# Kernel optimization log

Measured on AMD Instinct MI355X. Metric: run time of the kernel, lower is better.

Reference implementation:

```python
import jax, jax.numpy as jnp
import numpy as np
import math

V, E, H, NL = 10000, 256, 512, 2
B, T = 64, 128


def _lstm_cell(x, h, c, Wih, Whh, b):
    # PyTorch gate order: i, f, g, o
    gates = x @ Wih.T + h @ Whh.T + b
    i, f, g, o = jnp.split(gates, 4, axis=-1)
    c = jax.nn.sigmoid(f) * c + jax.nn.sigmoid(i) * jnp.tanh(g)
    h = jax.nn.sigmoid(o) * jnp.tanh(c)
    return h, c


def _run_layer(xs, Wih, Whh, b):
    # xs: [T, B, D]; returns outputs [T, B, H] and final (h, c)
    Bn = xs.shape[1]
    h0 = jnp.zeros((Bn, H), xs.dtype)
    c0 = jnp.zeros((Bn, H), xs.dtype)

    def step(carry, x):
        h, c = carry
        h, c = _lstm_cell(x, h, c, Wih, Whh, b)
        return (h, c), h

    (hT, cT), ys = jax.lax.scan(step, (h0, c0), xs)
    return ys, hT, cT


def setup_inputs() -> dict:
    key = jax.random.key(0)
    ks = jax.random.split(key, 24)
    s = 0.05

    def n(k, shape):
        return jax.random.normal(k, shape, dtype=jnp.float32) * s

    inp = {
        "input_ids": jax.random.randint(ks[0], (B, T), 0, V),
        "my_attention_mask": jax.random.randint(ks[1], (B, T), 0, 2),
        "update_step": 1000,
        # encoder params
        "enc_embed": n(ks[2], (V, E)),
        "enc_Wih0": n(ks[3], (4 * H, E)),
        "enc_Whh0": n(ks[4], (4 * H, H)),
        "enc_b0": n(ks[5], (4 * H,)),
        "enc_Wih1": n(ks[6], (4 * H, H)),
        "enc_Whh1": n(ks[7], (4 * H, H)),
        "enc_b1": n(ks[8], (4 * H,)),
        # decoder params
        "dec_embed": n(ks[9], (V, E)),
        "dec_Wih0": n(ks[10], (4 * H, E)),
        "dec_Whh0": n(ks[11], (4 * H, H)),
        "dec_b0": n(ks[12], (4 * H,)),
        "dec_Wih1": n(ks[13], (4 * H, H)),
        "dec_Whh1": n(ks[14], (4 * H, H)),
        "dec_b1": n(ks[15], (4 * H,)),
        "dec_Wout": n(ks[16], (V, H)),
        "dec_bout": n(ks[17], (V,)),
    }
    return inp


def _forward(input_ids, my_attention_mask, update_step,
             enc_embed, enc_Wih0, enc_Whh0, enc_b0, enc_Wih1, enc_Whh1, enc_b1,
             dec_embed, dec_Wih0, dec_Whh0, dec_b0, dec_Wih1, dec_Whh1, dec_b1,
             dec_Wout, dec_bout):
    temp_ids = input_ids.T                      # [T, B]
    mask = my_attention_mask                    # [B, T]

    # ---- encoder: 2-layer LSTM over the full sequence ----
    emb = enc_embed[temp_ids]                   # [T, B, E]
    ys0, h0, c0 = _run_layer(emb, enc_Wih0, enc_Whh0, enc_b0)
    _, h1, c1 = _run_layer(ys0, enc_Wih1, enc_Whh1, enc_b1)

    def dec_step(carry, tok):
        dh0, dc0, dh1, dc1 = carry
        x = dec_embed[tok]                      # [B, E]
        dh0, dc0 = _lstm_cell(x, dh0, dc0, dec_Wih0, dec_Whh0, dec_b0)
        dh1, dc1 = _lstm_cell(dh0, dh1, dc1, dec_Wih1, dec_Whh1, dec_b1)
        out = dh1 @ dec_Wout.T + dec_bout       # [B, V]
        return (dh0, dc0, dh1, dc1), out

    _, dec_outs = jax.lax.scan(dec_step, (h0, c0, h1, c1), temp_ids[:-1])  # [T-1, B, V]

    # ---- mask-driven compaction: outputs[i, j] = dec_out at t where
    #      i = exclusive-cumsum of mask[j, :t]; unwritten slots stay random ----
    outputs = jax.random.uniform(jax.random.key(42), (T, B, V), dtype=jnp.float32)
    idx = jnp.cumsum(mask, axis=1) - mask       # exclusive cumsum, [B, T]
    write_i = jnp.where(mask[:, 1:] > 0, idx[:, 1:], T)   # OOB -> dropped
    vals = jnp.transpose(dec_outs, (1, 0, 2))   # [B, T-1, V]
    outputs = outputs.at[write_i, jnp.arange(B)[:, None]].set(vals, mode="drop")

    # ---- hard gumbel-softmax with straight-through ----
    temperature = max(0.5, math.exp(-0.003 * update_step))
    eps = 1e-20
    U = jax.random.uniform(jax.random.key(7), (T, B, V), dtype=jnp.float32)
    g = -jnp.log(-jnp.log(U + eps) + eps)
    y = jax.nn.softmax((outputs + g) / temperature, axis=-1)
    y_hard = jax.nn.one_hot(jnp.argmax(y, axis=-1), V, dtype=y.dtype)
    gs = jax.lax.stop_gradient(y_hard - y) + y  # [T, B, V]

    # ---- scatter back into padded layout: masked positions pull compacted
    #      gumbel onehots, unmasked positions get onehot(input id) ----
    gathered = gs[jnp.clip(idx, 0, T - 1), jnp.arange(B)[:, None]]  # [B, T, V]
    id_onehot = jax.nn.one_hot(input_ids, V, dtype=jnp.float32)     # [B, T, V]
    onehots = jnp.where((mask > 0)[:, :, None], gathered, id_onehot)
    return onehots.reshape(B * T, V)


def reference(input_ids, my_attention_mask, update_step,
              enc_embed, enc_Wih0, enc_Whh0, enc_b0, enc_Wih1, enc_Whh1, enc_b1,
              dec_embed, dec_Wih0, dec_Whh0, dec_b0, dec_Wih1, dec_Whh1, dec_b1,
              dec_Wout, dec_bout):
    return _forward(input_ids, my_attention_mask, update_step,
                    enc_embed, enc_Wih0, enc_Whh0, enc_b0, enc_Wih1, enc_Whh1, enc_b1,
                    dec_embed, dec_Wih0, dec_Whh0, dec_b0, dec_Wih1, dec_Whh1, dec_b1,
                    dec_Wout, dec_bout)
```

## Files before the change

### kernel.cpp

```cpp
#include <hip/hip_runtime.h>
#include <stdint.h>


typedef short bf16x8 __attribute__((ext_vector_type(8)));
typedef float f32x4 __attribute__((ext_vector_type(4)));

__device__ __forceinline__ void threefry2x32(uint32_t k0, uint32_t k1,
                                             uint32_t x0, uint32_t x1,
                                             uint32_t& o0, uint32_t& o1)
{
  const uint32_t k2 = k0 ^ k1 ^ 0x1BD11BDAu;
  x0 += k0; x1 += k1;
#define TF_R(r) x0 += x1; x1 = (x1 << r) | (x1 >> (32 - r)); x1 ^= x0;
  TF_R(13) TF_R(15) TF_R(26) TF_R(6)
  x0 += k1; x1 += k2 + 1u;
  TF_R(17) TF_R(29) TF_R(16) TF_R(24)
  x0 += k2; x1 += k0 + 2u;
  TF_R(13) TF_R(15) TF_R(26) TF_R(6)
  x0 += k0; x1 += k1 + 3u;
  TF_R(17) TF_R(29) TF_R(16) TF_R(24)
  x0 += k1; x1 += k2 + 4u;
  TF_R(13) TF_R(15) TF_R(26) TF_R(6)
  x0 += k2; x1 += k0 + 5u;
#undef TF_R
  o0 = x0; o1 = x1;
}

__device__ __forceinline__ float jax_uniform(uint32_t seed, uint32_t i)
{
  uint32_t o0, o1;
  threefry2x32(0u, seed, 0u, i, o0, o1);
  const uint32_t bits = o0 ^ o1;
  return __uint_as_float(0x3F800000u | (bits >> 9)) - 1.0f;
}

__device__ __forceinline__ ushort f2bf(float x)
{
  const uint32_t u = __float_as_uint(x);
  const uint32_t r = u + 0x7FFFu + ((u >> 16) & 1u);
  return (ushort)(r >> 16);
}
__device__ __forceinline__ float bf2f(ushort b)
{
  return __uint_as_float(((uint32_t)b) << 16);
}

__device__ __forceinline__ unsigned long long packkey(float f, int n)
{
  uint32_t u = __float_as_uint(f);
  u = (u & 0x80000000u) ? ~u : (u | 0x80000000u);
  return ((unsigned long long)u << 32) | (uint32_t)(0x7FFFFFFF - n);
}

__global__ __launch_bounds__(256)
void split_kernel(const float* __restrict__ src, ushort* __restrict__ hi,
                  ushort* __restrict__ lo, int n)
{
  const int i = blockIdx.x * 256 + threadIdx.x;
  if (i < n) {
    const float v = src[i];
    const ushort h = f2bf(v);
    hi[i] = h;
    lo[i] = f2bf(v - bf2f(h));
  }
}

__global__ __launch_bounds__(256)
void transpose_split_kernel(const float* __restrict__ seq,
                            ushort* __restrict__ Thi, ushort* __restrict__ Tlo)
{
  __shared__ float tile[128][65];
  const int t = blockIdx.x >> 2;
  const int kc = blockIdx.x & 3;
  const int tid = threadIdx.x;
  const float* sbase = seq + (size_t)t * 32768 + (size_t)kc * 128 * 64;
#pragma unroll
  for (int it = 0; it < 32; ++it) {
    const int idx = it * 256 + tid;
    tile[idx >> 6][idx & 63] = sbase[idx];
  }
  __syncthreads();
#pragma unroll
  for (int it = 0; it < 32; ++it) {
    const int idx = it * 256 + tid;
    const int b = idx >> 7, k = idx & 127;
    const float v = tile[k][b];
    const size_t o = ((size_t)t * 64 + b) * 512 + kc * 128 + k;
    const ushort h = f2bf(v);
    Thi[o] = h;
    Tlo[o] = f2bf(v - bf2f(h));
  }
}

template <int GATHER, int FUSED>
__global__ __launch_bounds__(256)
void gemm_split(const ushort* __restrict__ Ahi, const ushort* __restrict__ Alo,
                const int* __restrict__ ids,
                const ushort* __restrict__ Whi, const ushort* __restrict__ Wlo,
                const float* __restrict__ bias, float* __restrict__ Xg,
                const int* __restrict__ mask, const int* __restrict__ idxmap,
                unsigned long long* __restrict__ keys,
                int M, int N, int K)
{
  const int tid = threadIdx.x;
  const int wid = tid >> 6, lane = tid & 63;
  const int lm = lane & 15, quad = lane >> 4;
  const int m0 = blockIdx.x * 128 + (wid >> 1) * 64;
  const int n0 = blockIdx.y * 128 + (wid & 1) * 64;
  const int koff = quad * 8;

  size_t offA[4];
#pragma unroll
  for (int mi = 0; mi < 4; ++mi) {
    int m = m0 + mi * 16 + lm;
    int mc = m < M ? m : (M - 1);
    if (GATHER) {
      const int tok = ids[(mc & 63) * 128 + (mc >> 6)];
      offA[mi] = (size_t)tok * K;
    } else {
      offA[mi] = (size_t)mc * K;
    }
  }
  size_t offB[4];
#pragma unroll
  for (int ni = 0; ni < 4; ++ni) {
    int n = n0 + ni * 16 + lm;
    int nc = n < N ? n : (N - 1);
    offB[ni] = (size_t)nc * K;
  }

  f32x4 acc[4][4];
#pragma unroll
  for (int mi = 0; mi < 4; ++mi)
#pragma unroll
    for (int ni = 0; ni < 4; ++ni) acc[mi][ni] = (f32x4){0.f, 0.f, 0.f, 0.f};

  for (int k0 = 0; k0 < K; k0 += 32) {
    bf16x8 ah[4], al[4];
#pragma unroll
    for (int mi = 0; mi < 4; ++mi) {
      ah[mi] = *(const bf16x8*)(Ahi + offA[mi] + k0 + koff);
      al[mi] = *(const bf16x8*)(Alo + offA[mi] + k0 + koff);
    }
#pragma unroll
    for (int ni = 0; ni < 4; ++ni) {
      const bf16x8 bh = *(const bf16x8*)(Whi + offB[ni] + k0 + koff);
      const bf16x8 bl = *(const bf16x8*)(Wlo + offB[ni] + k0 + koff);
#pragma unroll
      for (int mi = 0; mi < 4; ++mi) {
        acc[mi][ni] = __builtin_amdgcn_mfma_f32_16x16x32_bf16(ah[mi], bl, acc[mi][ni], 0, 0, 0);
        acc[mi][ni] = __builtin_amdgcn_mfma_f32_16x16x32_bf16(al[mi], bh, acc[mi][ni], 0, 0, 0);
        acc[mi][ni] = __builtin_amdgcn_mfma_f32_16x16x32_bf16(ah[mi], bh, acc[mi][ni], 0, 0, 0);
      }
    }
  }

  float bv[4];
#pragma unroll
  for (int ni = 0; ni < 4; ++ni) {
    int n = n0 + ni * 16 + lm;
    bv[ni] = bias[n < N ? n : (N - 1)];
  }

  if (FUSED == 0) {
#pragma unroll
    for (int mi = 0; mi < 4; ++mi) {
#pragma unroll
      for (int i = 0; i < 4; ++i) {
        const int m = m0 + mi * 16 + quad * 4 + i;
        if (m >= M) continue;
        const int t = m >> 6, b = m & 63;
        float* base = Xg + (size_t)t * 131072 + b;
#pragma unroll
        for (int ni = 0; ni < 4; ++ni) {
          const int n = n0 + ni * 16 + lm;
          base[(size_t)n * 64] = acc[mi][ni][i] + bv[ni];
        }
      }
    }
  } else {
#pragma unroll
    for (int mi = 0; mi < 4; ++mi) {
#pragma unroll
      for (int i = 0; i < 4; ++i) {
        const int m = m0 + mi * 16 + quad * 4 + i;
        if (m >= M) continue;
        const int j = m >> 6, b = m & 63;
        const int outrow = b * 128 + j + 1;
        if (mask[outrow] == 0) continue;
        const int r = idxmap[outrow];
        const uint32_t base7 = (uint32_t)(r * 64 + b) * 10000u;
        float best = -3.0e38f;
        int bestn = 0;
#pragma unroll
        for (int ni = 0; ni < 4; ++ni) {
          const int n = n0 + ni * 16 + lm;
          if (n < N) {
            const float u7 = jax_uniform(7u, base7 + (uint32_t)n);
            const float g = -logf(-logf(u7 + 1e-20f) + 1e-20f);
            const float z = acc[mi][ni][i] + bv[ni] + g;
            if (z > best) { best = z; bestn = n; }
          }
        }
        unsigned long long key = packkey(best, bestn);
#pragma unroll
        for (int s = 1; s < 16; s <<= 1) {
          const unsigned long long o = __shfl_xor(key, s, 64);
          if (o > key) key = o;
        }
        if (lm == 0) atomicMax(keys + outrow, key);
      }
    }
  }
}

__global__ __launch_bounds__(128)
void lstm_step_kernel(const float* __restrict__ Xg,
                      const float* __restrict__ hprev,
                      const float* __restrict__ Whh,
                      float* __restrict__ cstate,
                      float* __restrict__ hout)
{
  __shared__ __align__(16) float ws[8][512];
  __shared__ __align__(16) float hs[4096];
  const int tid = threadIdx.x;
  const int b = tid & 63;
  const int ui = tid >> 6;
  const int U0 = blockIdx.x * 2;
  const int u = U0 + ui;

  {
    const int r = tid >> 4;
    const int lui = r >> 2, lg = r & 3;
    const float* wrow = Whh + (size_t)(lg * 512 + U0 + lui) * 512;
    const int kq = tid & 15;
#pragma unroll
    for (int i = 0; i < 8; ++i) {
      const int k = kq * 4 + i * 64;
      *(float4*)&ws[r][k] = *(const float4*)(wrow + k);
    }
  }

  const float x_i = Xg[(size_t)(0 * 512 + u) * 64 + b];
  const float x_f = Xg[(size_t)(1 * 512 + u) * 64 + b];
  const float x_g = Xg[(size_t)(2 * 512 + u) * 64 + b];
  const float x_o = Xg[(size_t)(3 * 512 + u) * 64 + b];
  const float c_old = cstate[(size_t)u * 64 + b];

  float4 pre[8];
#pragma unroll
  for (int i = 0; i < 8; ++i) pre[i] = ((const float4*)hprev)[tid + 128 * i];

  float a0 = 0.f, a1 = 0.f, a2 = 0.f, a3 = 0.f;
  for (int kc = 0; kc < 8; ++kc) {
    __syncthreads();
#pragma unroll
    for (int i = 0; i < 8; ++i) ((float4*)hs)[tid + 128 * i] = pre[i];
    __syncthreads();
    if (kc < 7) {
#pragma unroll
      for (int i = 0; i < 8; ++i)
        pre[i] = ((const float4*)hprev)[(kc + 1) * 1024 + tid + 128 * i];
    }
    const int kb = kc * 64;
#pragma unroll
    for (int kg = 0; kg < 16; ++kg) {
      const float h0 = hs[(kg * 4 + 0) * 64 + b];
      const float h1 = hs[(kg * 4 + 1) * 64 + b];
      const float h2 = hs[(kg * 4 + 2) * 64 + b];
      const float h3 = hs[(kg * 4 + 3) * 64 + b];
      const float4 w0 = *(const float4*)&ws[ui * 4 + 0][kb + kg * 4];
      const float4 w1 = *(const float4*)&ws[ui * 4 + 1][kb + kg * 4];
      const float4 w2 = *(const float4*)&ws[ui * 4 + 2][kb + kg * 4];
      const float4 w3 = *(const float4*)&ws[ui * 4 + 3][kb + kg * 4];
      a0 += h0 * w0.x + h1 * w0.y + h2 * w0.z + h3 * w0.w;
      a1 += h0 * w1.x + h1 * w1.y + h2 * w1.z + h3 * w1.w;
      a2 += h0 * w2.x + h1 * w2.y + h2 * w2.z + h3 * w2.w;
      a3 += h0 * w3.x + h1 * w3.y + h2 * w3.z + h3 * w3.w;
    }
  }

  const float zi = x_i + a0, zf = x_f + a1, zg = x_g + a2, zo = x_o + a3;
  const float I = 1.0f / (1.0f + expf(-zi));
  const float F = 1.0f / (1.0f + expf(-zf));
  const float G = tanhf(zg);
  const float O = 1.0f / (1.0f + expf(-zo));
  const float cn = F * c_old + I * G;
  cstate[(size_t)u * 64 + b] = cn;
  hout[(size_t)u * 64 + b] = O * tanhf(cn);
}

__global__ void maskscan_kernel(const int* __restrict__ mask,
                                int* __restrict__ idxmap)
{
  const int b = threadIdx.x;
  int run = 0;
  for (int t = 0; t < 128; ++t) {
    idxmap[b * 128 + t] = run;
    run += mask[b * 128 + t];
  }
}

__global__ __launch_bounds__(256)
void t0_kernel(const int* __restrict__ mask, unsigned long long* __restrict__ keys)
{
  const int b = blockIdx.x;
  const int row = b * 128;
  if (mask[row] == 0) return;
  const int tid = threadIdx.x;
  const uint32_t base = (uint32_t)b * 10000u;
  float best = -3.0e38f;
  int bestn = 0;
  for (int v = tid; v < 10000; v += 256) {
    const float u42 = jax_uniform(42u, base + (uint32_t)v);
    const float u7 = jax_uniform(7u, base + (uint32_t)v);
    const float g = -logf(-logf(u7 + 1e-20f) + 1e-20f);
    const float z = u42 + g;
    if (z > best) { best = z; bestn = v; }
  }
  __shared__ unsigned long long sk[256];
  sk[tid] = packkey(best, bestn);
  __syncthreads();
  for (int s = 128; s > 0; s >>= 1) {
    if (tid < s) { if (sk[tid + s] > sk[tid]) sk[tid] = sk[tid + s]; }
    __syncthreads();
  }
  if (tid == 0) keys[row] = sk[0];
}

__global__ __launch_bounds__(256)
void finalize_kernel(const unsigned long long* __restrict__ keys,
                     const int* __restrict__ mask,
                     const int* __restrict__ input_ids,
                     int* __restrict__ tokens)
{
  const int row = blockIdx.x * 256 + threadIdx.x;
  if (row < 8192) {
    tokens[row] = mask[row] ? (int)(0x7FFFFFFFu - (uint32_t)(keys[row] & 0xFFFFFFFFu))
                            : input_ids[row];
  }
}

__global__ __launch_bounds__(256)
void onehot_kernel(const int* __restrict__ tokens, float* __restrict__ out)
{
  const int row = blockIdx.x;
  const int tok = tokens[row];
  float4* orow = (float4*)(out + (size_t)row * 10000);
  for (int q = threadIdx.x; q < 2500; q += 256) {
    float4 v = make_float4(0.f, 0.f, 0.f, 0.f);
    const int v0 = q << 2;
    const unsigned d = (unsigned)(tok - v0);
    if (d < 4u) ((float*)&v)[d] = 1.0f;
    orow[q] = v;
  }
}

__global__ __launch_bounds__(256)
void zero_kernel(float* __restrict__ p, int n)
{
  const int i = blockIdx.x * 256 + threadIdx.x;
  if (i < n) p[i] = 0.f;
}

extern "C" void kernel_launch(void* const* d_in, const int* in_sizes, int n_in,
                              void* d_out, int out_size, void* d_ws, size_t ws_size,
                              hipStream_t stream)
{
  const int*   input_ids = (const int*)d_in[0];
  const int*   mask      = (const int*)d_in[1];
  const float* enc_embed = (const float*)d_in[3];
  const float* enc_Wih0  = (const float*)d_in[4];
  const float* enc_Whh0  = (const float*)d_in[5];
  const float* enc_b0    = (const float*)d_in[6];
  const float* enc_Wih1  = (const float*)d_in[7];
  const float* enc_Whh1  = (const float*)d_in[8];
  const float* enc_b1    = (const float*)d_in[9];
  const float* dec_embed = (const float*)d_in[10];
  const float* dec_Wih0  = (const float*)d_in[11];
  const float* dec_Whh0  = (const float*)d_in[12];
  const float* dec_b0    = (const float*)d_in[13];
  const float* dec_Wih1  = (const float*)d_in[14];
  const float* dec_Whh1  = (const float*)d_in[15];
  const float* dec_b1    = (const float*)d_in[16];
  const float* dec_Wout  = (const float*)d_in[17];
  const float* dec_bout  = (const float*)d_in[18];

  char* O = (char*)d_out;
  float*  Xg    = (float*)(O + 0);
  ushort* sThi  = (ushort*)(O + 67108864);
  ushort* sTlo  = (ushort*)(O + 75497472);
  ushort* eEh   = (ushort*)(O + 83886080);
  ushort* eEl   = (ushort*)(O + 89006080);
  ushort* dEh   = (ushort*)(O + 94126080);
  ushort* dEl   = (ushort*)(O + 99246080);
  ushort* eW0h  = (ushort*)(O + 104366080);
  ushort* eW0l  = (ushort*)(O + 105414656);
  ushort* eW1h  = (ushort*)(O + 106463232);
  ushort* eW1l  = (ushort*)(O + 108560384);
  ushort* dW0h  = (ushort*)(O + 110657536);
  ushort* dW0l  = (ushort*)(O + 111706112);
  ushort* dW1h  = (ushort*)(O + 112754688);
  ushort* dW1l  = (ushort*)(O + 114851840);
  ushort* Woh   = (ushort*)(O + 116948992);
  ushort* Wol   = (ushort*)(O + 127188992);
  unsigned long long* keys = (unsigned long long*)(O + 137428992);
  int*    idxmap = (int*)(O + 137494528);

  float* seqA = (float*)d_ws;
  float* zbuf = seqA + (size_t)128 * 32768;
  float* cA   = zbuf + 32768;
  float* cB   = cA + 32768;
  float* hp0  = cB + 32768;
  float* hp1  = hp0 + 32768;
  int* tokens = (int*)(hp1 + 32768);

  zero_kernel<<<384, 256, 0, stream>>>(zbuf, 3 * 32768);
  zero_kernel<<<64, 256, 0, stream>>>((float*)keys, 16384);
  maskscan_kernel<<<1, 64, 0, stream>>>(mask, idxmap);

  split_kernel<<<10000, 256, 0, stream>>>(enc_embed, eEh, eEl, 2560000);
  split_kernel<<<10000, 256, 0, stream>>>(dec_embed, dEh, dEl, 2560000);
  split_kernel<<<2048, 256, 0, stream>>>(enc_Wih0, eW0h, eW0l, 524288);
  split_kernel<<<4096, 256, 0, stream>>>(enc_Wih1, eW1h, eW1l, 1048576);
  split_kernel<<<2048, 256, 0, stream>>>(dec_Wih0, dW0h, dW0l, 524288);
  split_kernel<<<4096, 256, 0, stream>>>(dec_Wih1, dW1h, dW1l, 1048576);
  split_kernel<<<20000, 256, 0, stream>>>(dec_Wout, Woh, Wol, 5120000);

  gemm_split<1, 0><<<dim3(64, 16), 256, 0, stream>>>(
      eEh, eEl, input_ids, eW0h, eW0l, enc_b0, Xg,
      nullptr, nullptr, nullptr, 8192, 2048, 256);
  for (int t = 0; t < 128; ++t) {
    const float* hi = (t == 0) ? zbuf : (seqA + (size_t)(t - 1) * 32768);
    lstm_step_kernel<<<256, 128, 0, stream>>>(
        Xg + (size_t)t * 131072, hi, enc_Whh0, cA, seqA + (size_t)t * 32768);
  }

  transpose_split_kernel<<<512, 256, 0, stream>>>(seqA, sThi, sTlo);
  gemm_split<0, 0><<<dim3(64, 16), 256, 0, stream>>>(
      sThi, sTlo, nullptr, eW1h, eW1l, enc_b1, Xg,
      nullptr, nullptr, nullptr, 8192, 2048, 512);
  for (int t = 0; t < 128; ++t) {
    const float* hi = (t == 0) ? zbuf : ((t & 1) ? hp0 : hp1);
    float* ho = (t & 1) ? hp1 : hp0;
    lstm_step_kernel<<<256, 128, 0, stream>>>(
        Xg + (size_t)t * 131072, hi, enc_Whh1, cB, ho);
  }

  gemm_split<1, 0><<<dim3(64, 16), 256, 0, stream>>>(
      dEh, dEl, input_ids, dW0h, dW0l, dec_b0, Xg,
      nullptr, nullptr, nullptr, 8128, 2048, 256);
  for (int j = 0; j < 127; ++j) {
    const float* hi = (j == 0) ? (seqA + (size_t)127 * 32768)
                               : (seqA + (size_t)(j - 1) * 32768);
    lstm_step_kernel<<<256, 128, 0, stream>>>(
        Xg + (size_t)j * 131072, hi, dec_Whh0, cA, seqA + (size_t)j * 32768);
  }

  transpose_split_kernel<<<508, 256, 0, stream>>>(seqA, sThi, sTlo);
  gemm_split<0, 0><<<dim3(64, 16), 256, 0, stream>>>(
      sThi, sTlo, nullptr, dW1h, dW1l, dec_b1, Xg,
      nullptr, nullptr, nullptr, 8128, 2048, 512);
  for (int j = 0; j < 127; ++j) {
    const float* hi = (j == 0) ? hp1 : (seqA + (size_t)(j - 1) * 32768);
    lstm_step_kernel<<<256, 128, 0, stream>>>(
        Xg + (size_t)j * 131072, hi, dec_Whh1, cB, seqA + (size_t)j * 32768);
  }

  transpose_split_kernel<<<508, 256, 0, stream>>>(seqA, sThi, sTlo);
  gemm_split<0, 1><<<dim3(64, 79), 256, 0, stream>>>(
      sThi, sTlo, nullptr, Woh, Wol, dec_bout, nullptr,
      mask, idxmap, keys, 8128, 10000, 512);
  t0_kernel<<<64, 256, 0, stream>>>(mask, keys);

  finalize_kernel<<<32, 256, 0, stream>>>(keys, mask, input_ids, tokens);
  onehot_kernel<<<8192, 256, 0, stream>>>(tokens, (float*)d_out);
}
```

Baseline: 12.06 ms.

## Replace FP32 LSTM recurrent step with split-bf16 MFMA kernel using ping-pong hidden buffers

The recurrent h@Whh product in each LSTM timestep moves from an FP32 shared-memory dot-product kernel to a kernel using bf16 MFMA with a hi/lo split (three MFMAs per tile) to keep near-FP32 accuracy. Whh matrices are pre-split into bf16 hi/lo once, and each step writes its hidden state in a batch-major bf16 hi/lo layout into ping-pong buffers read by the next step. The kernel uses 32 blocks of 256 threads instead of 256 blocks of 128, so far fewer workgroups are used per step, which reduces parallelism across the GPU. There are also extra split launches and an extra per-step write of the hidden state.

```diff
diff --git a/kernel.cpp b/kernel.cpp
--- a/kernel.cpp
+++ b/kernel.cpp
@@ -214,80 +214,80 @@
   }
 }
 
-__global__ __launch_bounds__(128)
-void lstm_step_kernel(const float* __restrict__ Xg,
-                      const float* __restrict__ hprev,
-                      const float* __restrict__ Whh,
-                      float* __restrict__ cstate,
-                      float* __restrict__ hout)
-{
-  __shared__ __align__(16) float ws[8][512];
-  __shared__ __align__(16) float hs[4096];
+__global__ __launch_bounds__(256)
+void lstm_step_mfma(const float* __restrict__ Xg,
+                    const ushort* __restrict__ hHi, const ushort* __restrict__ hLo,
+                    const ushort* __restrict__ WHi, const ushort* __restrict__ WLo,
+                    float* __restrict__ cstate, float* __restrict__ hout,
+                    ushort* __restrict__ oHi, ushort* __restrict__ oLo)
+{
   const int tid = threadIdx.x;
-  const int b = tid & 63;
-  const int ui = tid >> 6;
-  const int U0 = blockIdx.x * 2;
-  const int u = U0 + ui;
-
-  {
-    const int r = tid >> 4;
-    const int lui = r >> 2, lg = r & 3;
-    const float* wrow = Whh + (size_t)(lg * 512 + U0 + lui) * 512;
-    const int kq = tid & 15;
-#pragma unroll
-    for (int i = 0; i < 8; ++i) {
-      const int k = kq * 4 + i * 64;
-      *(float4*)&ws[r][k] = *(const float4*)(wrow + k);
+  const int mi = tid >> 6;
+  const int lane = tid & 63;
+  const int lm = lane & 15, quad = lane >> 4;
+  const int u = blockIdx.x * 16 + lm;
+  const int koff = quad * 8;
+
+  const ushort* aHi = hHi + (size_t)(mi * 16 + lm) * 512 + koff;
+  const ushort* aLo = hLo + (size_t)(mi * 16 + lm) * 512 + koff;
+  const ushort* bH[4];
+  const ushort* bL[4];
+#pragma unroll
+  for (int g = 0; g < 4; ++g) {
+    const size_t o = (size_t)(g * 512 + u) * 512 + koff;
+    bH[g] = WHi + o;
+    bL[g] = WLo + o;
+  }
+
+  f32x4 acc[4];
+#pragma unroll
+  for (int g = 0; g < 4; ++g) acc[g] = (f32x4){0.f, 0.f, 0.f, 0.f};
+
+#pragma unroll 4
+  for (int k0 = 0; k0 < 512; k0 += 32) {
+    const bf16x8 ah = *(const bf16x8*)(aHi + k0);
+    const bf16x8 al = *(const bf16x8*)(aLo + k0);
+#pragma unroll
+    for (int g = 0; g < 4; ++g) {
+      const bf16x8 bh = *(const bf16x8*)(bH[g] + k0);
+      const bf16x8 bl = *(const bf16x8*)(bL[g] + k0);
+      acc[g] = __builtin_amdgcn_mfma_f32_16x16x32_bf16(ah, bl, acc[g], 0, 0, 0);
+      acc[g] = __builtin_amdgcn_mfma_f32_16x16x32_bf16(al, bh, acc[g], 0, 0, 0);
+      acc[g] = __builtin_amdgcn_mfma_f32_16x16x32_bf16(ah, bh, acc[g], 0, 0, 0);
     }
   }
 
-  const float x_i = Xg[(size_t)(0 * 512 + u) * 64 + b];
-  const float x_f = Xg[(size_t)(1 * 512 + u) * 64 + b];
-  const float x_g = Xg[(size_t)(2 * 512 + u) * 64 + b];
-  const float x_o = Xg[(size_t)(3 * 512 + u) * 64 + b];
-  const float c_old = cstate[(size_t)u * 64 + b];
-
-  float4 pre[8];
-#pragma unroll
-  for (int i = 0; i < 8; ++i) pre[i] = ((const float4*)hprev)[tid + 128 * i];
-
-  float a0 = 0.f, a1 = 0.f, a2 = 0.f, a3 = 0.f;
-  for (int kc = 0; kc < 8; ++kc) {
-    __syncthreads();
-#pragma unroll
-    for (int i = 0; i < 8; ++i) ((float4*)hs)[tid + 128 * i] = pre[i];
-    __syncthreads();
-    if (kc < 7) {
-#pragma unroll
-      for (int i = 0; i < 8; ++i)
-        pre[i] = ((const float4*)hprev)[(kc + 1) * 1024 + tid + 128 * i];
-    }
-    const int kb = kc * 64;
-#pragma unroll
-    for (int kg = 0; kg < 16; ++kg) {
-      const float h0 = hs[(kg * 4 + 0) * 64 + b];
-      const float h1 = hs[(kg * 4 + 1) * 64 + b];
-      const float h2 = hs[(kg * 4 + 2) * 64 + b];
-      const float h3 = hs[(kg * 4 + 3) * 64 + b];
-      const float4 w0 = *(const float4*)&ws[ui * 4 + 0][kb + kg * 4];
-      const float4 w1 = *(const float4*)&ws[ui * 4 + 1][kb + kg * 4];
-      const float4 w2 = *(const float4*)&ws[ui * 4 + 2][kb + kg * 4];
-      const float4 w3 = *(const float4*)&ws[ui * 4 + 3][kb + kg * 4];
-      a0 += h0 * w0.x + h1 * w0.y + h2 * w0.z + h3 * w0.w;
-      a1 += h0 * w1.x + h1 * w1.y + h2 * w1.z + h3 * w1.w;
-      a2 += h0 * w2.x + h1 * w2.y + h2 * w2.z + h3 * w2.w;
-      a3 += h0 * w3.x + h1 * w3.y + h2 * w3.z + h3 * w3.w;
-    }
-  }
-
-  const float zi = x_i + a0, zf = x_f + a1, zg = x_g + a2, zo = x_o + a3;
-  const float I = 1.0f / (1.0f + expf(-zi));
-  const float F = 1.0f / (1.0f + expf(-zf));
-  const float G = tanhf(zg);
-  const float O = 1.0f / (1.0f + expf(-zo));
-  const float cn = F * c_old + I * G;
-  cstate[(size_t)u * 64 + b] = cn;
-  hout[(size_t)u * 64 + b] = O * tanhf(cn);
+  const int b0 = mi * 16 + quad * 4;
+  const float4 xi = *(const float4*)(Xg + (size_t)(0 * 512 + u) * 64 + b0);
+  const float4 xf = *(const float4*)(Xg + (size_t)(1 * 512 + u) * 64 + b0);
+  const float4 xg = *(const float4*)(Xg + (size_t)(2 * 512 + u) * 64 + b0);
+  const float4 xo = *(const float4*)(Xg + (size_t)(3 * 512 + u) * 64 + b0);
+  float4 c4 = *(float4*)(cstate + (size_t)u * 64 + b0);
+
+  float4 h4;
+#pragma unroll
+  for (int r = 0; r < 4; ++r) {
+    const float zi = acc[0][r] + ((const float*)&xi)[r];
+    const float zf = acc[1][r] + ((const float*)&xf)[r];
+    const float zg = acc[2][r] + ((const float*)&xg)[r];
+    const float zo = acc[3][r] + ((const float*)&xo)[r];
+    const float I = 1.0f / (1.0f + expf(-zi));
+    const float F = 1.0f / (1.0f + expf(-zf));
+    const float G = tanhf(zg);
+    const float O = 1.0f / (1.0f + expf(-zo));
+    const float cn = F * ((float*)&c4)[r] + I * G;
+    ((float*)&c4)[r] = cn;
+    ((float*)&h4)[r] = O * tanhf(cn);
+  }
+  *(float4*)(cstate + (size_t)u * 64 + b0) = c4;
+  *(float4*)(hout + (size_t)u * 64 + b0) = h4;
+#pragma unroll
+  for (int r = 0; r < 4; ++r) {
+    const float hv = ((const float*)&h4)[r];
+    const ushort hh = f2bf(hv);
+    oHi[(size_t)(b0 + r) * 512 + u] = hh;
+    oLo[(size_t)(b0 + r) * 512 + u] = f2bf(hv - bf2f(hh));
+  }
 }
 
 __global__ void maskscan_kernel(const int* __restrict__ mask,
@@ -406,6 +406,22 @@
   ushort* Wol   = (ushort*)(O + 127188992);
   unsigned long long* keys = (unsigned long long*)(O + 137428992);
   int*    idxmap = (int*)(O + 137494528);
+  ushort* eH0h = (ushort*)(O + 137527296);
+  ushort* eH0l = (ushort*)(O + 139624448);
+  ushort* eH1h = (ushort*)(O + 141721600);
+  ushort* eH1l = (ushort*)(O + 143818752);
+  ushort* dH0h = (ushort*)(O + 145915904);
+  ushort* dH0l = (ushort*)(O + 148013056);
+  ushort* dH1h = (ushort*)(O + 150110208);
+  ushort* dH1l = (ushort*)(O + 152207360);
+  ushort* hsAhi = (ushort*)(O + 154304512);
+  ushort* hsAlo = (ushort*)(O + 154370048);
+  ushort* hsBhi = (ushort*)(O + 154435584);
+  ushort* hsBlo = (ushort*)(O + 154501120);
+  ushort* hsChi = (ushort*)(O + 154566656);
+  ushort* hsClo = (ushort*)(O + 154632192);
+  ushort* hsDhi = (ushort*)(O + 154697728);
+  ushort* hsDlo = (ushort*)(O + 154763264);
 
   float* seqA = (float*)d_ws;
   float* zbuf = seqA + (size_t)128 * 32768;
@@ -415,7 +431,8 @@
   float* hp1  = hp0 + 32768;
   int* tokens = (int*)(hp1 + 32768);
 
-  zero_kernel<<<384, 256, 0, stream>>>(zbuf, 3 * 32768);
+  zero_kernel<<<256, 256, 0, stream>>>(cA, 2 * 32768);
+  zero_kernel<<<512, 256, 0, stream>>>((float*)hsAhi, 131072);
   zero_kernel<<<64, 256, 0, stream>>>((float*)keys, 16384);
   maskscan_kernel<<<1, 64, 0, stream>>>(mask, idxmap);
 
@@ -426,14 +443,22 @@
   split_kernel<<<2048, 256, 0, stream>>>(dec_Wih0, dW0h, dW0l, 524288);
   split_kernel<<<4096, 256, 0, stream>>>(dec_Wih1, dW1h, dW1l, 1048576);
   split_kernel<<<20000, 256, 0, stream>>>(dec_Wout, Woh, Wol, 5120000);
+  split_kernel<<<4096, 256, 0, stream>>>(enc_Whh0, eH0h, eH0l, 1048576);
+  split_kernel<<<4096, 256, 0, stream>>>(enc_Whh1, eH1h, eH1l, 1048576);
+  split_kernel<<<4096, 256, 0, stream>>>(dec_Whh0, dH0h, dH0l, 1048576);
+  split_kernel<<<4096, 256, 0, stream>>>(dec_Whh1, dH1h, dH1l, 1048576);
 
   gemm_split<1, 0><<<dim3(64, 16), 256, 0, stream>>>(
       eEh, eEl, input_ids, eW0h, eW0l, enc_b0, Xg,
       nullptr, nullptr, nullptr, 8192, 2048, 256);
   for (int t = 0; t < 128; ++t) {
-    const float* hi = (t == 0) ? zbuf : (seqA + (size_t)(t - 1) * 32768);
-    lstm_step_kernel<<<256, 128, 0, stream>>>(
-        Xg + (size_t)t * 131072, hi, enc_Whh0, cA, seqA + (size_t)t * 32768);
+    const ushort* ih = (t & 1) ? hsBhi : hsAhi;
+    const ushort* il = (t & 1) ? hsBlo : hsAlo;
+    ushort* oh = (t & 1) ? hsAhi : hsBhi;
+    ushort* ol = (t & 1) ? hsAlo : hsBlo;
+    lstm_step_mfma<<<32, 256, 0, stream>>>(
+        Xg + (size_t)t * 131072, ih, il, eH0h, eH0l, cA,
+        seqA + (size_t)t * 32768, oh, ol);
   }
 
   transpose_split_kernel<<<512, 256, 0, stream>>>(seqA, sThi, sTlo);
@@ -441,20 +466,25 @@
       sThi, sTlo, nullptr, eW1h, eW1l, enc_b1, Xg,
       nullptr, nullptr, nullptr, 8192, 2048, 512);
   for (int t = 0; t < 128; ++t) {
-    const float* hi = (t == 0) ? zbuf : ((t & 1) ? hp0 : hp1);
-    float* ho = (t & 1) ? hp1 : hp0;
-    lstm_step_kernel<<<256, 128, 0, stream>>>(
-        Xg + (size_t)t * 131072, hi, enc_Whh1, cB, ho);
+    const ushort* ih = (t & 1) ? hsDhi : hsChi;
+    const ushort* il = (t & 1) ? hsDlo : hsClo;
+    ushort* oh = (t & 1) ? hsChi : hsDhi;
+    ushort* ol = (t & 1) ? hsClo : hsDlo;
+    lstm_step_mfma<<<32, 256, 0, stream>>>(
+        Xg + (size_t)t * 131072, ih, il, eH1h, eH1l, cB, hp0, oh, ol);
   }
 
   gemm_split<1, 0><<<dim3(64, 16), 256, 0, stream>>>(
       dEh, dEl, input_ids, dW0h, dW0l, dec_b0, Xg,
       nullptr, nullptr, nullptr, 8128, 2048, 256);
   for (int j = 0; j < 127; ++j) {
-    const float* hi = (j == 0) ? (seqA + (size_t)127 * 32768)
-                               : (seqA + (size_t)(j - 1) * 32768);
-    lstm_step_kernel<<<256, 128, 0, stream>>>(
-        Xg + (size_t)j * 131072, hi, dec_Whh0, cA, seqA + (size_t)j * 32768);
+    const ushort* ih = (j & 1) ? hsBhi : hsAhi;
+    const ushort* il = (j & 1) ? hsBlo : hsAlo;
+    ushort* oh = (j & 1) ? hsAhi : hsBhi;
+    ushort* ol = (j & 1) ? hsAlo : hsBlo;
+    lstm_step_mfma<<<32, 256, 0, stream>>>(
+        Xg + (size_t)j * 131072, ih, il, dH0h, dH0l, cA,
+        seqA + (size_t)j * 32768, oh, ol);
   }
 
   transpose_split_kernel<<<508, 256, 0, stream>>>(seqA, sThi, sTlo);
@@ -462,9 +492,13 @@
       sThi, sTlo, nullptr, dW1h, dW1l, dec_b1, Xg,
       nullptr, nullptr, nullptr, 8128, 2048, 512);
   for (int j = 0; j < 127; ++j) {
-    const float* hi = (j == 0) ? hp1 : (seqA + (size_t)(j - 1) * 32768);
-    lstm_step_kernel<<<256, 128, 0, stream>>>(
-        Xg + (size_t)j * 131072, hi, dec_Whh1, cB, seqA + (size_t)j * 32768);
+    const ushort* ih = (j & 1) ? hsDhi : hsChi;
+    const ushort* il = (j & 1) ? hsDlo : hsClo;
+    ushort* oh = (j & 1) ? hsChi : hsDhi;
+    ushort* ol = (j & 1) ? hsClo : hsDlo;
+    lstm_step_mfma<<<32, 256, 0, stream>>>(
+        Xg + (size_t)j * 131072, ih, il, dH1h, dH1l, cB,
+        seqA + (size_t)j * 32768, oh, ol);
   }
 
   transpose_split_kernel<<<508, 256, 0, stream>>>(seqA, sThi, sTlo);
```

Result: slower. 13.05 ms (+8.2%).
